# Kernel optimization log

Hardware: AMD Instinct MI355X
Metric: run time of the kernel (lower is better)

Reference implementation:

```python
import jax, jax.numpy as jnp
import numpy as np

B_, DIM, NPTS = 16, 128, 16384
J, K, L = 16, 128, 128   # kernel_mode, GkNN_mode_out, GkNN_mode_in
R, M1, M2 = 8, 64, 64    # low-rank A/B dims and mask modes


def setup_inputs() -> dict:
    key = jax.random.key(0)
    ks = jax.random.split(key, 9)
    scale = 1.0 / (L * K)
    return {
        "x": jax.random.normal(ks[0], (B_, DIM, NPTS), jnp.float32),
        "bases": jax.random.normal(ks[1], (NPTS, K), jnp.float32),
        "wbases": jax.random.normal(ks[2], (NPTS, L), jnp.float32),
        "product": jax.random.normal(ks[3], (K, L), jnp.float32),
        "D_out": jax.random.normal(ks[4], (J, K), jnp.float32),
        "D_in": jax.random.normal(ks[5], (J, L), jnp.float32),
        "A": jax.random.normal(ks[6], (J, R, M1), jnp.float32),
        "B": jax.random.normal(ks[7], (J, R, M2), jnp.float32),
        "weights": scale * jax.random.normal(ks[8], (DIM, DIM, J), jnp.float32),
    }


def reference(x, bases, wbases, product, D_out, D_in, A, B, weights):
    # project onto weighted bases: (b, c, npts) @ (npts, L) -> (b, c, L)
    x_hat = jnp.einsum('bcx,xl->bcl', x, wbases)
    # H tensor: (J, K, L) broadcast product + low-rank correction
    H = D_out[:, :, None] * D_in[:, None, :] * product[None, :, :]
    Q = jnp.einsum('jrm,jrn->jmn', A, B)  # bmm(A^T, B): (J, M1, M2)
    H = H.at[:, :Q.shape[1], :Q.shape[2]].add(Q)
    # mode mixing: (J,K,L) x (b,i,L) -> (b,i,J,K), then weights (i,o,J)
    x_hat1 = jnp.einsum('jkl,bil->bijk', H, x_hat)
    y = jnp.einsum('ioj,bijk->bok', weights, x_hat1)
    # back to physical space: (b, o, K) x (npts, K) -> (b, o, npts)
    return jnp.einsum('bok,xk->box', y, bases)
```

## Files before the change

### kernel.cpp

```cpp
#include <hip/hip_runtime.h>

#define B_    16
#define DIM   128
#define NPTS  16384
#define J_    16
#define K_    128
#define L_    128
#define R_    8
#define M1_   64

typedef float  f32x4 __attribute__((ext_vector_type(4)));
typedef short  s16x8 __attribute__((ext_vector_type(8)));
typedef unsigned short u16;
typedef u16 u16x8 __attribute__((ext_vector_type(8)));
typedef u16 u16x4 __attribute__((ext_vector_type(4)));

__device__ __forceinline__ u16 f2bf(float f) {
    unsigned u = __float_as_uint(f);
    u += 0x7FFFu + ((u >> 16) & 1u);
    return (u16)(u >> 16);
}
#define MFMA16(a,b,c) __builtin_amdgcn_mfma_f32_16x16x32_bf16((a),(b),(c),0,0,0)

#define OFF_PARTA 0u
#define OFF_WBT   8388608u
#define OFF_BASB  12582912u
#define OFF_HKL   16777216u
#define OFF_W2T   17301504u
#define OFF_XHB   17825792u
#define OFF_YB    18350080u
#define OFF_YP    18874368u

__global__ __launch_bounds__(256) void k_prep(
    const float* __restrict__ product, const float* __restrict__ Do,
    const float* __restrict__ Di, const float* __restrict__ A,
    const float* __restrict__ Bm, const float* __restrict__ W,
    const float* __restrict__ wb, const float* __restrict__ bases,
    u16* __restrict__ Hkl, u16* __restrict__ W2T,
    u16* __restrict__ wbT, u16* __restrict__ basesb)
{
    __shared__ u16 sT[128][136];
    const int bid = blockIdx.x, t = threadIdx.x;
    if (bid < 1024) {
        int idx = (bid << 8) | t;
        int j = idx >> 14, k = (idx >> 7) & 127, l = idx & 127;
        float v = Do[j*K_ + k] * Di[j*L_ + l] * product[k*L_ + l];
        if (k < M1_ && l < M1_) {
            float q = 0.f;
            #pragma unroll
            for (int r = 0; r < R_; ++r)
                q += A[(j*R_ + r)*M1_ + k] * Bm[(j*R_ + r)*M1_ + l];
            v += q;
        }
        Hkl[idx] = f2bf(v);
    } else if (bid < 2048) {
        int idx = ((bid - 1024) << 8) | t;
        int o = idx >> 11, ji = idx & 2047, j = ji >> 7, i = ji & 127;
        W2T[idx] = f2bf(W[(i*DIM + o)*J_ + j]);
    } else if (bid < 2176) {
        const int p0 = (bid - 2048) * 128;
        #pragma unroll
        for (int it = 0; it < 16; ++it) {
            int idx = it*256 + t, row = idx >> 5, c4 = (idx & 31) * 4;
            float4 v = *(const float4*)(wb + (size_t)(p0+row)*L_ + c4);
            sT[c4+0][row] = f2bf(v.x); sT[c4+1][row] = f2bf(v.y);
            sT[c4+2][row] = f2bf(v.z); sT[c4+3][row] = f2bf(v.w);
        }
        __syncthreads();
        #pragma unroll
        for (int it = 0; it < 8; ++it) {
            int idx = it*256 + t, l = idx >> 4, pc = (idx & 15) * 8;
            *(u16x8*)(wbT + (size_t)l*NPTS + p0 + pc) = *(const u16x8*)&sT[l][pc];
        }
    } else {
        int i = (((bid - 2176) << 8) | t) * 4;
        float4 v = *(const float4*)(bases + i);
        u16x4 o4 = { f2bf(v.x), f2bf(v.y), f2bf(v.z), f2bf(v.w) };
        *(u16x4*)(basesb + i) = o4;
    }
}

__global__ __launch_bounds__(512) void k_stageA(
    const float* __restrict__ x, const u16* __restrict__ wbT,
    float* __restrict__ part)
{
    __shared__ u16 sA[64][136];
    __shared__ u16 sB[128][136];
    const int t = threadIdx.x, lane = t & 63, wave = t >> 6;
    const int quad = lane >> 4, l16 = lane & 15;
    const int wr = wave >> 2, wc = wave & 3;
    const int m0 = blockIdx.x * 64;
    const size_t pbase = (size_t)blockIdx.y * 2048;

    f32x4 acc[2][2] = {};
    const int ac4 = (t & 31) * 4, arr = t >> 5;
    const int bc8 = (t & 15) * 8, brr = t >> 4;

    for (int pc = 0; pc < 2048; pc += 128) {
        #pragma unroll
        for (int i = 0; i < 4; ++i) {
            int row = arr + 16*i;
            float4 v = *(const float4*)(x + (size_t)(m0+row)*NPTS + pbase + pc + ac4);
            u16x4 h = { f2bf(v.x), f2bf(v.y), f2bf(v.z), f2bf(v.w) };
            *(u16x4*)&sA[row][ac4] = h;
        }
        #pragma unroll
        for (int i = 0; i < 4; ++i) {
            int row = brr + 32*i;
            *(u16x8*)&sB[row][bc8] =
                *(const u16x8*)(wbT + (size_t)row*NPTS + pbase + pc + bc8);
        }
        __syncthreads();
        #pragma unroll
        for (int ks = 0; ks < 4; ++ks) {
            int kb = ks*32 + quad*8;
            s16x8 a0 = *(const s16x8*)&sA[wr*32      + l16][kb];
            s16x8 a1 = *(const s16x8*)&sA[wr*32 + 16 + l16][kb];
            s16x8 b0 = *(const s16x8*)&sB[wc*32      + l16][kb];
            s16x8 b1 = *(const s16x8*)&sB[wc*32 + 16 + l16][kb];
            acc[0][0] = MFMA16(a0, b0, acc[0][0]);
            acc[0][1] = MFMA16(a0, b1, acc[0][1]);
            acc[1][0] = MFMA16(a1, b0, acc[1][0]);
            acc[1][1] = MFMA16(a1, b1, acc[1][1]);
        }
        __syncthreads();
    }
    float* po = part + (size_t)blockIdx.y * (2048*128);
    #pragma unroll
    for (int mt = 0; mt < 2; ++mt)
      #pragma unroll
      for (int r = 0; r < 4; ++r) {
        int row = m0 + wr*32 + mt*16 + quad*4 + r;
        #pragma unroll
        for (int nt = 0; nt < 2; ++nt) {
            int col = wc*32 + nt*16 + l16;
            po[(size_t)row*128 + col] = acc[mt][nt][r];
        }
      }
}

__global__ __launch_bounds__(256) void k_reduceA(
    const float* __restrict__ part, u16* __restrict__ xhatb)
{
    int i = blockIdx.x * 1024 + threadIdx.x;
    #pragma unroll
    for (int e = 0; e < 4; ++e, i += 256) {
        float s = 0.f;
        #pragma unroll
        for (int p = 0; p < 8; ++p) s += part[p*262144 + i];
        xhatb[i] = f2bf(s);
    }
}

__global__ __launch_bounds__(256) void k_mix1(
    const u16* __restrict__ Hkl, const u16* __restrict__ xhatb,
    u16* __restrict__ Tt)
{
    __shared__ u16 sA[128][136];
    __shared__ u16 sB[128][136];
    const int t = threadIdx.x, lane = t & 63, wave = t >> 6;
    const int quad = lane >> 4, l16 = lane & 15;
    const int wr = wave >> 1, wc = wave & 1;
    const int b = blockIdx.x, j = blockIdx.y;
    const u16* ha = Hkl + j*16384;
    const u16* xb = xhatb + b*16384;

    const int c8 = (t & 15)*8, rr = t >> 4;
    #pragma unroll
    for (int i = 0; i < 8; ++i) {
        int row = rr + 16*i;
        *(u16x8*)&sA[row][c8] = *(const u16x8*)(ha + row*128 + c8);
        *(u16x8*)&sB[row][c8] = *(const u16x8*)(xb + row*128 + c8);
    }
    __syncthreads();

    f32x4 acc[4][4] = {};
    #pragma unroll
    for (int ks = 0; ks < 4; ++ks) {
        int kb = ks*32 + quad*8;
        s16x8 a[4], bf[4];
        #pragma unroll
        for (int mt = 0; mt < 4; ++mt) a[mt]  = *(const s16x8*)&sA[wr*64 + mt*16 + l16][kb];
        #pragma unroll
        for (int nt = 0; nt < 4; ++nt) bf[nt] = *(const s16x8*)&sB[wc*64 + nt*16 + l16][kb];
        #pragma unroll
        for (int mt = 0; mt < 4; ++mt)
            #pragma unroll
            for (int nt = 0; nt < 4; ++nt)
                acc[mt][nt] = MFMA16(a[mt], bf[nt], acc[mt][nt]);
    }
    u16* to = Tt + (size_t)b*262144 + (j << 7);
    #pragma unroll
    for (int mt = 0; mt < 4; ++mt)
      #pragma unroll
      for (int r = 0; r < 4; ++r) {
        int k = wr*64 + mt*16 + quad*4 + r;
        #pragma unroll
        for (int nt = 0; nt < 4; ++nt) {
            int i = wc*64 + nt*16 + l16;
            to[(size_t)k*2048 + i] = f2bf(acc[mt][nt][r]);
        }
      }
}

__global__ __launch_bounds__(256) void k_mix2(
    const u16* __restrict__ W2T, const u16* __restrict__ Tt,
    float* __restrict__ ypart)
{
    __shared__ u16 sA[128][136];
    __shared__ u16 sB[128][136];
    const int t = threadIdx.x, lane = t & 63, wave = t >> 6;
    const int quad = lane >> 4, l16 = lane & 15;
    const int wr = wave >> 1, wc = wave & 1;
    const int b = blockIdx.x, c = blockIdx.y;
    const int ji0 = c * 128;
    const u16* tb = Tt + (size_t)b*262144;

    const int c8 = (t & 15)*8, rr = t >> 4;
    #pragma unroll
    for (int i = 0; i < 8; ++i) {
        int row = rr + 16*i;
        *(u16x8*)&sA[row][c8] = *(const u16x8*)(W2T + (size_t)row*2048 + ji0 + c8);
        *(u16x8*)&sB[row][c8] = *(const u16x8*)(tb  + (size_t)row*2048 + ji0 + c8);
    }
    __syncthreads();

    f32x4 acc[4][4] = {};
    #pragma unroll
    for (int ks = 0; ks < 4; ++ks) {
        int kb = ks*32 + quad*8;
        s16x8 a[4], bf[4];
        #pragma unroll
        for (int mt = 0; mt < 4; ++mt) a[mt]  = *(const s16x8*)&sA[wr*64 + mt*16 + l16][kb];
        #pragma unroll
        for (int nt = 0; nt < 4; ++nt) bf[nt] = *(const s16x8*)&sB[wc*64 + nt*16 + l16][kb];
        #pragma unroll
        for (int mt = 0; mt < 4; ++mt)
            #pragma unroll
            for (int nt = 0; nt < 4; ++nt)
                acc[mt][nt] = MFMA16(a[mt], bf[nt], acc[mt][nt]);
    }
    float* yo = ypart + ((size_t)(c*16 + b) << 14);
    #pragma unroll
    for (int mt = 0; mt < 4; ++mt)
      #pragma unroll
      for (int r = 0; r < 4; ++r) {
        int o = wr*64 + mt*16 + quad*4 + r;
        #pragma unroll
        for (int nt = 0; nt < 4; ++nt) {
            int k = wc*64 + nt*16 + l16;
            yo[(size_t)o*128 + k] = acc[mt][nt][r];
        }
      }
}

__global__ __launch_bounds__(256) void k_reduceY(
    const float* __restrict__ part, u16* __restrict__ yb)
{
    int i = blockIdx.x * 1024 + threadIdx.x;
    #pragma unroll
    for (int e = 0; e < 4; ++e, i += 256) {
        float s = 0.f;
        #pragma unroll
        for (int p = 0; p < 16; ++p) s += part[p*262144 + i];
        yb[i] = f2bf(s);
    }
}

__global__ __launch_bounds__(256) void k_stageE(
    const u16* __restrict__ yb, const u16* __restrict__ basesb,
    float* __restrict__ out)
{
    __shared__ u16 sA[128][136];
    __shared__ u16 sB[128][136];
    const int t = threadIdx.x, lane = t & 63, wave = t >> 6;
    const int quad = lane >> 4, l16 = lane & 15;
    const int wr = wave >> 1, wc = wave & 1;
    const int bo0 = blockIdx.x * 128, p0 = blockIdx.y * 128;

    const int c8 = (t & 15)*8, rr = t >> 4;
    #pragma unroll
    for (int i = 0; i < 8; ++i) {
        int row = rr + 16*i;
        *(u16x8*)&sA[row][c8] = *(const u16x8*)(yb     + (size_t)(bo0+row)*128 + c8);
        *(u16x8*)&sB[row][c8] = *(const u16x8*)(basesb + (size_t)(p0 +row)*128 + c8);
    }
    __syncthreads();

    f32x4 acc[4][4] = {};
    #pragma unroll
    for (int ks = 0; ks < 4; ++ks) {
        int kb = ks*32 + quad*8;
        s16x8 a[4], bf[4];
        #pragma unroll
        for (int mt = 0; mt < 4; ++mt) a[mt]  = *(const s16x8*)&sA[wr*64 + mt*16 + l16][kb];
        #pragma unroll
        for (int nt = 0; nt < 4; ++nt) bf[nt] = *(const s16x8*)&sB[wc*64 + nt*16 + l16][kb];
        #pragma unroll
        for (int mt = 0; mt < 4; ++mt)
            #pragma unroll
            for (int nt = 0; nt < 4; ++nt)
                acc[mt][nt] = MFMA16(a[mt], bf[nt], acc[mt][nt]);
    }
    #pragma unroll
    for (int mt = 0; mt < 4; ++mt)
      #pragma unroll
      for (int r = 0; r < 4; ++r) {
        size_t row = bo0 + wr*64 + mt*16 + quad*4 + r;
        #pragma unroll
        for (int nt = 0; nt < 4; ++nt) {
            int p = p0 + wc*64 + nt*16 + l16;
            out[row*NPTS + p] = acc[mt][nt][r];
        }
      }
}

extern "C" void kernel_launch(void* const* d_in, const int* in_sizes, int n_in,
                              void* d_out, int out_size, void* d_ws, size_t ws_size,
                              hipStream_t stream) {
    (void)in_sizes; (void)n_in; (void)out_size; (void)ws_size;
    const float* x       = (const float*)d_in[0];
    const float* bases   = (const float*)d_in[1];
    const float* wbases  = (const float*)d_in[2];
    const float* product = (const float*)d_in[3];
    const float* Do      = (const float*)d_in[4];
    const float* Di      = (const float*)d_in[5];
    const float* A       = (const float*)d_in[6];
    const float* Bm      = (const float*)d_in[7];
    const float* W       = (const float*)d_in[8];

    char* ws = (char*)d_ws;
    float* partA  = (float*)(ws + OFF_PARTA);
    u16*   Tt     = (u16*)  (ws + OFF_PARTA);
    u16*   wbT    = (u16*)  (ws + OFF_WBT);
    u16*   basesb = (u16*)  (ws + OFF_BASB);
    u16*   Hkl    = (u16*)  (ws + OFF_HKL);
    u16*   W2T    = (u16*)  (ws + OFF_W2T);
    u16*   xhatb  = (u16*)  (ws + OFF_XHB);
    u16*   yb     = (u16*)  (ws + OFF_YB);
    float* ypart  = (float*)(ws + OFF_YP);

    k_prep   <<<4224, 256, 0, stream>>>(product, Do, Di, A, Bm, W, wbases, bases,
                                        Hkl, W2T, wbT, basesb);
    k_stageA <<<dim3(32, 8), 512, 0, stream>>>(x, wbT, partA);
    k_reduceA<<<256, 256, 0, stream>>>(partA, xhatb);
    k_mix1   <<<dim3(16, 16), 256, 0, stream>>>(Hkl, xhatb, Tt);
    k_mix2   <<<dim3(16, 16), 256, 0, stream>>>(W2T, Tt, ypart);
    k_reduceY<<<256, 256, 0, stream>>>(ypart, yb);
    k_stageE <<<dim3(16, 128), 256, 0, stream>>>(yb, basesb, (float*)d_out);
}
```

Baseline: 315.6 us.

## Fuse mix kernels, prefetch stageA tiles in registers, convert bases inside stageE

The two mode-mixing GEMMs are merged into one kernel. The intermediate (k,i) tile for each (b,j) stays in shared memory and is multiplied by that j's weight slice there, so the Tt global round trip goes away. The per-j partial outputs are now written as bf16, and the reduce kernel reads them with 8-wide vectors, which halves partial traffic but adds rounding error across the 16-way sum. StageA now prefetches the next chunk of x and wbT into registers while the MFMAs run, and the fp32 bases are converted to bf16 inside stageE instead of in a separate prep pass.

```diff
diff --git a/kernel.cpp b/kernel.cpp
--- a/kernel.cpp
+++ b/kernel.cpp
@@ -20,24 +20,25 @@
     u += 0x7FFFu + ((u >> 16) & 1u);
     return (u16)(u >> 16);
 }
+__device__ __forceinline__ float bf2f(u16 h) {
+    return __uint_as_float(((unsigned)h) << 16);
+}
 #define MFMA16(a,b,c) __builtin_amdgcn_mfma_f32_16x16x32_bf16((a),(b),(c),0,0,0)
 
 #define OFF_PARTA 0u
 #define OFF_WBT   8388608u
-#define OFF_BASB  12582912u
-#define OFF_HKL   16777216u
-#define OFF_W2T   17301504u
-#define OFF_XHB   17825792u
-#define OFF_YB    18350080u
-#define OFF_YP    18874368u
+#define OFF_HKL   12582912u
+#define OFF_W2T   13107200u
+#define OFF_XHB   13631488u
+#define OFF_YB    14155776u
+#define OFF_YPB   14680064u
 
 __global__ __launch_bounds__(256) void k_prep(
     const float* __restrict__ product, const float* __restrict__ Do,
     const float* __restrict__ Di, const float* __restrict__ A,
     const float* __restrict__ Bm, const float* __restrict__ W,
-    const float* __restrict__ wb, const float* __restrict__ bases,
-    u16* __restrict__ Hkl, u16* __restrict__ W2T,
-    u16* __restrict__ wbT, u16* __restrict__ basesb)
+    const float* __restrict__ wb,
+    u16* __restrict__ Hkl, u16* __restrict__ W2T, u16* __restrict__ wbT)
 {
     __shared__ u16 sT[128][136];
     const int bid = blockIdx.x, t = threadIdx.x;
@@ -57,7 +58,7 @@
         int idx = ((bid - 1024) << 8) | t;
         int o = idx >> 11, ji = idx & 2047, j = ji >> 7, i = ji & 127;
         W2T[idx] = f2bf(W[(i*DIM + o)*J_ + j]);
-    } else if (bid < 2176) {
+    } else {
         const int p0 = (bid - 2048) * 128;
         #pragma unroll
         for (int it = 0; it < 16; ++it) {
@@ -72,11 +73,6 @@
             int idx = it*256 + t, l = idx >> 4, pc = (idx & 15) * 8;
             *(u16x8*)(wbT + (size_t)l*NPTS + p0 + pc) = *(const u16x8*)&sT[l][pc];
         }
-    } else {
-        int i = (((bid - 2176) << 8) | t) * 4;
-        float4 v = *(const float4*)(bases + i);
-        u16x4 o4 = { f2bf(v.x), f2bf(v.y), f2bf(v.z), f2bf(v.w) };
-        *(u16x4*)(basesb + i) = o4;
     }
 }
 
@@ -96,21 +92,29 @@
     const int ac4 = (t & 31) * 4, arr = t >> 5;
     const int bc8 = (t & 15) * 8, brr = t >> 4;
 
+    float4 ra[4];
+    u16x8  rb[4];
+    #pragma unroll
+    for (int i = 0; i < 4; ++i) {
+        ra[i] = *(const float4*)(x + (size_t)(m0 + arr + 16*i)*NPTS + pbase + ac4);
+        rb[i] = *(const u16x8*)(wbT + (size_t)(brr + 32*i)*NPTS + pbase + bc8);
+    }
+
     for (int pc = 0; pc < 2048; pc += 128) {
         #pragma unroll
         for (int i = 0; i < 4; ++i) {
-            int row = arr + 16*i;
-            float4 v = *(const float4*)(x + (size_t)(m0+row)*NPTS + pbase + pc + ac4);
-            u16x4 h = { f2bf(v.x), f2bf(v.y), f2bf(v.z), f2bf(v.w) };
-            *(u16x4*)&sA[row][ac4] = h;
-        }
-        #pragma unroll
-        for (int i = 0; i < 4; ++i) {
-            int row = brr + 32*i;
-            *(u16x8*)&sB[row][bc8] =
-                *(const u16x8*)(wbT + (size_t)row*NPTS + pbase + pc + bc8);
+            u16x4 h = { f2bf(ra[i].x), f2bf(ra[i].y), f2bf(ra[i].z), f2bf(ra[i].w) };
+            *(u16x4*)&sA[arr + 16*i][ac4] = h;
+            *(u16x8*)&sB[brr + 32*i][bc8] = rb[i];
         }
         __syncthreads();
+        if (pc + 128 < 2048) {
+            #pragma unroll
+            for (int i = 0; i < 4; ++i) {
+                ra[i] = *(const float4*)(x + (size_t)(m0 + arr + 16*i)*NPTS + pbase + pc + 128 + ac4);
+                rb[i] = *(const u16x8*)(wbT + (size_t)(brr + 32*i)*NPTS + pbase + pc + 128 + bc8);
+            }
+        }
         #pragma unroll
         for (int ks = 0; ks < 4; ++ks) {
             int kb = ks*32 + quad*8;
@@ -152,9 +156,9 @@
     }
 }
 
-__global__ __launch_bounds__(256) void k_mix1(
+__global__ __launch_bounds__(256) void k_mixF(
     const u16* __restrict__ Hkl, const u16* __restrict__ xhatb,
-    u16* __restrict__ Tt)
+    const u16* __restrict__ W2T, u16* __restrict__ ypartb)
 {
     __shared__ u16 sA[128][136];
     __shared__ u16 sB[128][136];
@@ -174,7 +178,7 @@
     }
     __syncthreads();
 
-    f32x4 acc[4][4] = {};
+    f32x4 acc1[4][4] = {};
     #pragma unroll
     for (int ks = 0; ks < 4; ++ks) {
         int kb = ks*32 + quad*8;
@@ -187,60 +191,42 @@
         for (int mt = 0; mt < 4; ++mt)
             #pragma unroll
             for (int nt = 0; nt < 4; ++nt)
-                acc[mt][nt] = MFMA16(a[mt], bf[nt], acc[mt][nt]);
-    }
-    u16* to = Tt + (size_t)b*262144 + (j << 7);
+                acc1[mt][nt] = MFMA16(a[mt], bf[nt], acc1[mt][nt]);
+    }
+    __syncthreads();
+
     #pragma unroll
     for (int mt = 0; mt < 4; ++mt)
       #pragma unroll
       for (int r = 0; r < 4; ++r) {
         int k = wr*64 + mt*16 + quad*4 + r;
         #pragma unroll
-        for (int nt = 0; nt < 4; ++nt) {
-            int i = wc*64 + nt*16 + l16;
-            to[(size_t)k*2048 + i] = f2bf(acc[mt][nt][r]);
-        }
+        for (int nt = 0; nt < 4; ++nt)
+            sA[k][wc*64 + nt*16 + l16] = f2bf(acc1[mt][nt][r]);
       }
-}
-
-__global__ __launch_bounds__(256) void k_mix2(
-    const u16* __restrict__ W2T, const u16* __restrict__ Tt,
-    float* __restrict__ ypart)
-{
-    __shared__ u16 sA[128][136];
-    __shared__ u16 sB[128][136];
-    const int t = threadIdx.x, lane = t & 63, wave = t >> 6;
-    const int quad = lane >> 4, l16 = lane & 15;
-    const int wr = wave >> 1, wc = wave & 1;
-    const int b = blockIdx.x, c = blockIdx.y;
-    const int ji0 = c * 128;
-    const u16* tb = Tt + (size_t)b*262144;
-
-    const int c8 = (t & 15)*8, rr = t >> 4;
     #pragma unroll
     for (int i = 0; i < 8; ++i) {
         int row = rr + 16*i;
-        *(u16x8*)&sA[row][c8] = *(const u16x8*)(W2T + (size_t)row*2048 + ji0 + c8);
-        *(u16x8*)&sB[row][c8] = *(const u16x8*)(tb  + (size_t)row*2048 + ji0 + c8);
+        *(u16x8*)&sB[row][c8] = *(const u16x8*)(W2T + (size_t)row*2048 + j*128 + c8);
     }
     __syncthreads();
 
-    f32x4 acc[4][4] = {};
+    f32x4 acc2[4][4] = {};
     #pragma unroll
     for (int ks = 0; ks < 4; ++ks) {
         int kb = ks*32 + quad*8;
         s16x8 a[4], bf[4];
         #pragma unroll
-        for (int mt = 0; mt < 4; ++mt) a[mt]  = *(const s16x8*)&sA[wr*64 + mt*16 + l16][kb];
-        #pragma unroll
-        for (int nt = 0; nt < 4; ++nt) bf[nt] = *(const s16x8*)&sB[wc*64 + nt*16 + l16][kb];
+        for (int mt = 0; mt < 4; ++mt) a[mt]  = *(const s16x8*)&sB[wr*64 + mt*16 + l16][kb];
+        #pragma unroll
+        for (int nt = 0; nt < 4; ++nt) bf[nt] = *(const s16x8*)&sA[wc*64 + nt*16 + l16][kb];
         #pragma unroll
         for (int mt = 0; mt < 4; ++mt)
             #pragma unroll
             for (int nt = 0; nt < 4; ++nt)
-                acc[mt][nt] = MFMA16(a[mt], bf[nt], acc[mt][nt]);
-    }
-    float* yo = ypart + ((size_t)(c*16 + b) << 14);
+                acc2[mt][nt] = MFMA16(a[mt], bf[nt], acc2[mt][nt]);
+    }
+    u16* yo = ypartb + ((size_t)(j*16 + b) << 14);
     #pragma unroll
     for (int mt = 0; mt < 4; ++mt)
       #pragma unroll
@@ -249,26 +235,30 @@
         #pragma unroll
         for (int nt = 0; nt < 4; ++nt) {
             int k = wc*64 + nt*16 + l16;
-            yo[(size_t)o*128 + k] = acc[mt][nt][r];
+            yo[(size_t)o*128 + k] = f2bf(acc2[mt][nt][r]);
         }
       }
 }
 
 __global__ __launch_bounds__(256) void k_reduceY(
-    const float* __restrict__ part, u16* __restrict__ yb)
-{
-    int i = blockIdx.x * 1024 + threadIdx.x;
-    #pragma unroll
-    for (int e = 0; e < 4; ++e, i += 256) {
-        float s = 0.f;
-        #pragma unroll
-        for (int p = 0; p < 16; ++p) s += part[p*262144 + i];
-        yb[i] = f2bf(s);
-    }
+    const u16* __restrict__ part, u16* __restrict__ yb)
+{
+    int i8 = (blockIdx.x * 256 + threadIdx.x) * 8;
+    float s[8] = {};
+    #pragma unroll
+    for (int p = 0; p < 16; ++p) {
+        u16x8 v = *(const u16x8*)(part + p*262144 + i8);
+        #pragma unroll
+        for (int e = 0; e < 8; ++e) s[e] += bf2f(v[e]);
+    }
+    u16x8 o;
+    #pragma unroll
+    for (int e = 0; e < 8; ++e) o[e] = f2bf(s[e]);
+    *(u16x8*)(yb + i8) = o;
 }
 
 __global__ __launch_bounds__(256) void k_stageE(
-    const u16* __restrict__ yb, const u16* __restrict__ basesb,
+    const u16* __restrict__ yb, const float* __restrict__ bases,
     float* __restrict__ out)
 {
     __shared__ u16 sA[128][136];
@@ -282,8 +272,15 @@
     #pragma unroll
     for (int i = 0; i < 8; ++i) {
         int row = rr + 16*i;
-        *(u16x8*)&sA[row][c8] = *(const u16x8*)(yb     + (size_t)(bo0+row)*128 + c8);
-        *(u16x8*)&sB[row][c8] = *(const u16x8*)(basesb + (size_t)(p0 +row)*128 + c8);
+        *(u16x8*)&sA[row][c8] = *(const u16x8*)(yb + (size_t)(bo0+row)*128 + c8);
+    }
+    const int c4 = (t & 31) * 4, br = t >> 5;
+    #pragma unroll
+    for (int i = 0; i < 16; ++i) {
+        int row = br + 8*i;
+        float4 v = *(const float4*)(bases + (size_t)(p0+row)*K_ + c4);
+        u16x4 h = { f2bf(v.x), f2bf(v.y), f2bf(v.z), f2bf(v.w) };
+        *(u16x4*)&sB[row][c4] = h;
     }
     __syncthreads();
 
@@ -331,21 +328,18 @@
 
     char* ws = (char*)d_ws;
     float* partA  = (float*)(ws + OFF_PARTA);
-    u16*   Tt     = (u16*)  (ws + OFF_PARTA);
     u16*   wbT    = (u16*)  (ws + OFF_WBT);
-    u16*   basesb = (u16*)  (ws + OFF_BASB);
     u16*   Hkl    = (u16*)  (ws + OFF_HKL);
     u16*   W2T    = (u16*)  (ws + OFF_W2T);
     u16*   xhatb  = (u16*)  (ws + OFF_XHB);
     u16*   yb     = (u16*)  (ws + OFF_YB);
-    float* ypart  = (float*)(ws + OFF_YP);
-
-    k_prep   <<<4224, 256, 0, stream>>>(product, Do, Di, A, Bm, W, wbases, bases,
-                                        Hkl, W2T, wbT, basesb);
+    u16*   ypartb = (u16*)  (ws + OFF_YPB);
+
+    k_prep   <<<2176, 256, 0, stream>>>(product, Do, Di, A, Bm, W, wbases,
+                                        Hkl, W2T, wbT);
     k_stageA <<<dim3(32, 8), 512, 0, stream>>>(x, wbT, partA);
     k_reduceA<<<256, 256, 0, stream>>>(partA, xhatb);
-    k_mix1   <<<dim3(16, 16), 256, 0, stream>>>(Hkl, xhatb, Tt);
-    k_mix2   <<<dim3(16, 16), 256, 0, stream>>>(W2T, Tt, ypart);
-    k_reduceY<<<256, 256, 0, stream>>>(ypart, yb);
-    k_stageE <<<dim3(16, 128), 256, 0, stream>>>(yb, basesb, (float*)d_out);
-}
+    k_mixF   <<<dim3(16, 16), 256, 0, stream>>>(Hkl, xhatb, W2T, ypartb);
+    k_reduceY<<<128, 256, 0, stream>>>(ypartb, yb);
+    k_stageE <<<dim3(16, 128), 256, 0, stream>>>(yb, bases, (float*)d_out);
+}
```

After: 319.9 us. Within noise of the previous version (+1.4%).
